# Kernel optimization log

Measured on AMD Instinct MI355X. Metric: run time of the kernel, lower is better.

## Reference

```python
import jax, jax.numpy as jnp
import numpy as np

N, D_IN, D_QK, D_V = 8192, 1024, 128, 128

def setup_inputs() -> dict:
    key = jax.random.key(0)
    k1, k2, k3, k4 = jax.random.split(key, 4)
    return {
        "x": jax.random.normal(k1, (N, D_IN), dtype=jnp.float32),
        "W_q": jax.random.normal(k2, (D_IN, D_QK), dtype=jnp.float32),
        "W_k": jax.random.normal(k3, (D_IN, D_QK), dtype=jnp.float32),
        "W_v": jax.random.normal(k4, (D_IN, D_V), dtype=jnp.float32),
    }

def reference(x, W_q, W_k, W_v):
    Q = x @ W_q          # [N, d_qk]
    K = x @ W_k          # [N, d_qk]
    V = x @ W_v          # [N, d_v]
    scale = 1.0 / jnp.sqrt(jnp.asarray(W_q.shape[1], dtype=Q.dtype))
    S = jnp.einsum("nd,md->nm", Q, K) * scale  # [N, N]
    A = jax.nn.softmax(S, axis=1)
    return A @ V         # [N, d_v]
```

## Files before the change

### kernel.cpp

```cpp
#include <hip/hip_runtime.h>
#include <cstdint>
#include <cstddef>

#define NTOK 8192
#define DIN  1024
#define DH   128
#define KVB  64

typedef __attribute__((ext_vector_type(4))) float f32x4;
typedef __bf16 bf16x8 __attribute__((ext_vector_type(8)));
typedef unsigned short u16x8 __attribute__((ext_vector_type(8)));
typedef unsigned short u16x4 __attribute__((ext_vector_type(4)));

__device__ __forceinline__ unsigned short f2bf(float f){
  union { float f; unsigned u; } x; x.f = f;
  unsigned r = x.u + 0x7FFFu + ((x.u >> 16) & 1u);
  return (unsigned short)(r >> 16);
}
__device__ __forceinline__ float bf2f(unsigned short b){
  union { unsigned u; float f; } x; x.u = ((unsigned)b) << 16;
  return x.f;
}
__device__ __forceinline__ void gload16(const void* g, void* l){
  using gp_t = const __attribute__((address_space(1))) char*;
  using lp_t = __attribute__((address_space(3))) char*;
  __builtin_amdgcn_global_load_lds((gp_t)(uintptr_t)g, (lp_t)(uint32_t)(uintptr_t)l, 16, 0, 0);
}

__global__ void k_wsplit(const float* __restrict__ Wq, const float* __restrict__ Wk,
                         const float* __restrict__ Wv,
                         unsigned short* __restrict__ WhT, unsigned short* __restrict__ WlT){
  int e = blockIdx.x * 256 + threadIdx.x;
  int n = e >> 10, k = e & 1023;
  const float* W = (n < 128) ? Wq : ((n < 256) ? Wk : Wv);
  float v = W[(size_t)k * 128 + (n & 127)];
  unsigned short h = f2bf(v);
  WhT[e] = h;
  WlT[e] = f2bf(v - bf2f(h));
}

__global__ void k_xsplit(const float* __restrict__ x,
                         unsigned short* __restrict__ xh, unsigned short* __restrict__ xl){
  size_t i = ((size_t)blockIdx.x * 256 + threadIdx.x) * 8;
  f32x4 a = *(const f32x4*)(x + i);
  f32x4 b = *(const f32x4*)(x + i + 4);
  u16x8 h, l;
  #pragma unroll
  for (int j = 0; j < 4; ++j){
    unsigned short h0 = f2bf(a[j]); h[j] = h0;   l[j]   = f2bf(a[j] - bf2f(h0));
    unsigned short h1 = f2bf(b[j]); h[4+j] = h1; l[4+j] = f2bf(b[j] - bf2f(h1));
  }
  *(u16x8*)(xh + i) = h;
  *(u16x8*)(xl + i) = l;
}

__global__ __launch_bounds__(256, 3) void k_proj(
    const unsigned short* __restrict__ xh, const unsigned short* __restrict__ xl,
    const unsigned short* __restrict__ WhT, const unsigned short* __restrict__ WlT,
    unsigned short* __restrict__ Qh, unsigned short* __restrict__ Ql,
    unsigned short* __restrict__ Kh, unsigned short* __restrict__ Kl,
    unsigned short* __restrict__ Vt){
  __shared__ __align__(16) char smem[32768];
  const int lane = threadIdx.x & 63, wid = threadIdx.x >> 6;
  const int l15 = lane & 15, lk = lane >> 4;
  const int bm = blockIdx.x;
  const int by = blockIdx.y;
  const int bt = by >> 1, nh = by & 1;
  const int wm = wid >> 1, wn = wid & 1;

  const int srow = lane >> 3;
  const int gc8  = (lane & 7) ^ srow;
  const unsigned short* gsrc;
  char* ldst;
  int grow0;
  if (wid == 0){      gsrc = xh;  grow0 = bm*64;            ldst = smem; }
  else if (wid == 1){ gsrc = xl;  grow0 = bm*64;            ldst = smem + 8192; }
  else if (wid == 2){ gsrc = WhT; grow0 = bt*128 + nh*64;   ldst = smem + 16384; }
  else {              gsrc = WlT; grow0 = bt*128 + nh*64;   ldst = smem + 24576; }
  const unsigned short* gbase = gsrc + (size_t)(grow0 + srow)*DIN + gc8*8;
  const bool stage_on = (bt < 2) || (wid == 0) || (wid == 2);

  f32x4 acc[2][2] = {};

  for (int t = 0; t < 16; ++t){
    if (stage_on){
      #pragma unroll
      for (int i = 0; i < 8; ++i)
        gload16(gbase + (size_t)i*8*DIN + t*64, ldst + i*1024);
    }
    __syncthreads();

    bf16x8 a_h[2][2], a_l[2][2], b_h[2][2], b_l[2][2];
    const unsigned sw = (unsigned)(l15 & 7);
    #pragma unroll
    for (int mf = 0; mf < 2; ++mf)
      #pragma unroll
      for (int kc = 0; kc < 2; ++kc){
        unsigned rA = (unsigned)(wm*32 + mf*16 + l15);
        unsigned offA = rA*128u + ((((unsigned)(kc*4 + lk)) ^ sw)*16u);
        a_h[mf][kc] = *(const bf16x8*)(const void*)(smem + offA);
        unsigned rB = (unsigned)(wn*32 + mf*16 + l15);
        unsigned offB = rB*128u + ((((unsigned)(kc*4 + lk)) ^ sw)*16u);
        b_h[mf][kc] = *(const bf16x8*)(const void*)(smem + 16384 + offB);
        if (bt < 2){
          a_l[mf][kc] = *(const bf16x8*)(const void*)(smem + 8192 + offA);
          b_l[mf][kc] = *(const bf16x8*)(const void*)(smem + 24576 + offB);
        }
      }
    #pragma unroll
    for (int mf = 0; mf < 2; ++mf)
      #pragma unroll
      for (int nf = 0; nf < 2; ++nf)
        #pragma unroll
        for (int kc = 0; kc < 2; ++kc){
          acc[mf][nf] = __builtin_amdgcn_mfma_f32_16x16x32_bf16(a_h[mf][kc], b_h[nf][kc], acc[mf][nf], 0,0,0);
          if (bt < 2){
            acc[mf][nf] = __builtin_amdgcn_mfma_f32_16x16x32_bf16(a_h[mf][kc], b_l[nf][kc], acc[mf][nf], 0,0,0);
            acc[mf][nf] = __builtin_amdgcn_mfma_f32_16x16x32_bf16(a_l[mf][kc], b_h[nf][kc], acc[mf][nf], 0,0,0);
          }
        }
    __syncthreads();
  }

  const float qscale = 0.08838834764831845f;
  #pragma unroll
  for (int mf = 0; mf < 2; ++mf){
    #pragma unroll
    for (int nf = 0; nf < 2; ++nf){
      #pragma unroll
      for (int r = 0; r < 4; ++r){
        int row = bm*64 + wm*32 + mf*16 + lk*4 + r;
        int col = nh*64 + wn*32 + nf*16 + l15;
        float v = acc[mf][nf][r];
        if (bt == 0){
          v *= qscale;
          unsigned short h = f2bf(v);
          Qh[(size_t)row*DH + col] = h;
          Ql[(size_t)row*DH + col] = f2bf(v - bf2f(h));
        } else if (bt == 1){
          unsigned short h = f2bf(v);
          Kh[(size_t)row*DH + col] = h;
          Kl[(size_t)row*DH + col] = f2bf(v - bf2f(h));
        } else {
          Vt[(size_t)col*NTOK + row] = f2bf(v);
        }
      }
    }
  }
}

__global__ __launch_bounds__(512, 4) void k_flash(
    const unsigned short* __restrict__ Qh, const unsigned short* __restrict__ Ql,
    const unsigned short* __restrict__ Kh, const unsigned short* __restrict__ Kl,
    const unsigned short* __restrict__ Vt,
    float* __restrict__ Opart, float* __restrict__ mpart, float* __restrict__ lpart,
    int ksplit){
  __shared__ __align__(16) char smem[65536];
  const int tid = threadIdx.x;
  const int lane = tid & 63, wid = tid >> 6;
  const int l15 = lane & 15, lk = lane >> 4;
  const int qb = blockIdx.x / ksplit, ks = blockIdx.x - qb*ksplit;
  const int q0 = qb*128 + wid*16;
  const int kvlen = NTOK / ksplit;
  const int kvbase = ks * kvlen;
  const int NT = kvlen / KVB;

  char* Pbase = smem + 48*1024 + wid*2048;

  bf16x8 qh[4], ql[4];
  #pragma unroll
  for (int kc = 0; kc < 4; ++kc){
    size_t off = (size_t)(q0 + l15)*DH + kc*32 + lk*8;
    qh[kc] = *(const bf16x8*)(const void*)(Qh + off);
    ql[kc] = *(const bf16x8*)(const void*)(Ql + off);
  }

  const int i0 = 2*wid, i1 = 2*wid + 1;
  int rk0 = 4*i0 + (lane >> 4), rk1 = 4*i1 + (lane >> 4);
  int gk0 = rk0*DH + ((lane & 15) ^ (rk0 & 7))*8;
  int gk1 = rk1*DH + ((lane & 15) ^ (rk1 & 7))*8;
  int rv0 = 8*i0 + (lane >> 3), rv1 = 8*i1 + (lane >> 3);
  int gv0 = rv0*NTOK + ((lane & 7) ^ (rv0 & 7))*8;
  int gv1 = rv1*NTOK + ((lane & 7) ^ (rv1 & 7))*8;
  char* ldsK0 = smem + i0*1024;
  char* ldsK1 = smem + i1*1024;

  #define STAGE(kv0_) do {                                              \
    int _o = (kv0_)*DH;                                                 \
    gload16(Kh + (size_t)(_o + gk0), ldsK0);                            \
    gload16(Kh + (size_t)(_o + gk1), ldsK1);                            \
    gload16(Kl + (size_t)(_o + gk0), ldsK0 + 16*1024);                  \
    gload16(Kl + (size_t)(_o + gk1), ldsK1 + 16*1024);                  \
    gload16(Vt + (size_t)(gv0 + (kv0_)), ldsK0 + 32*1024);              \
    gload16(Vt + (size_t)(gv1 + (kv0_)), ldsK1 + 32*1024);              \
  } while(0)

  STAGE(kvbase);
  __syncthreads();

  f32x4 o[8] = {};
  float m_run = -3.0e38f, l_run = 0.f;

  for (int t = 0; t < NT; ++t){
    f32x4 s[4] = {};
    __builtin_amdgcn_s_setprio(1);
    #pragma unroll
    for (int nf = 0; nf < 4; ++nf){
      const int row = nf*16 + l15;
      const unsigned rbase = (unsigned)row*256u;
      const unsigned sw = (unsigned)(row & 7);
      #pragma unroll
      for (int kc = 0; kc < 4; ++kc){
        unsigned boff = rbase + ((((unsigned)(kc*4 + lk)) ^ sw)*16u);
        bf16x8 khf = *(const bf16x8*)(const void*)(smem + boff);
        bf16x8 klf = *(const bf16x8*)(const void*)(smem + 16*1024 + boff);
        s[nf] = __builtin_amdgcn_mfma_f32_16x16x32_bf16(khf, qh[kc], s[nf], 0,0,0);
        s[nf] = __builtin_amdgcn_mfma_f32_16x16x32_bf16(klf, qh[kc], s[nf], 0,0,0);
        s[nf] = __builtin_amdgcn_mfma_f32_16x16x32_bf16(khf, ql[kc], s[nf], 0,0,0);
      }
    }
    __builtin_amdgcn_s_setprio(0);

    float mx = fmaxf(fmaxf(s[0][0], s[0][1]), fmaxf(s[0][2], s[0][3]));
    #pragma unroll
    for (int nf = 1; nf < 4; ++nf)
      mx = fmaxf(mx, fmaxf(fmaxf(s[nf][0], s[nf][1]), fmaxf(s[nf][2], s[nf][3])));
    mx = fmaxf(mx, __shfl_xor(mx, 16));
    mx = fmaxf(mx, __shfl_xor(mx, 32));
    float mnew = fmaxf(m_run, mx);
    float corr = __expf(m_run - mnew);
    float tsum = 0.f;
    #pragma unroll
    for (int nf = 0; nf < 4; ++nf){
      u16x4 pk;
      #pragma unroll
      for (int r = 0; r < 4; ++r){
        float p = __expf(s[nf][r] - mnew);
        tsum += p;
        pk[r] = f2bf(p);
      }
      *(u16x4*)(void*)(Pbase + l15*128 + (((unsigned)(nf*4 + lk)) ^ (2u*(unsigned)(l15 & 7)))*8u) = pk;
    }
    tsum += __shfl_xor(tsum, 16);
    tsum += __shfl_xor(tsum, 32);
    m_run = mnew;
    l_run = l_run*corr + tsum;
    #pragma unroll
    for (int nd = 0; nd < 8; ++nd) o[nd] *= corr;

    __builtin_amdgcn_s_setprio(1);
    #pragma unroll
    for (int kc2 = 0; kc2 < 2; ++kc2){
      bf16x8 pf = *(const bf16x8*)(const void*)(Pbase + l15*128 +
                    ((((unsigned)(kc2*4 + lk)) ^ (unsigned)(l15 & 7))*16u));
      #pragma unroll
      for (int nd = 0; nd < 8; ++nd){
        const int row = nd*16 + l15;
        unsigned boff = 32u*1024u + (unsigned)row*128u +
                        ((((unsigned)(kc2*4 + lk)) ^ (unsigned)(row & 7))*16u);
        bf16x8 vf = *(const bf16x8*)(const void*)(smem + boff);
        o[nd] = __builtin_amdgcn_mfma_f32_16x16x32_bf16(vf, pf, o[nd], 0,0,0);
      }
    }
    __builtin_amdgcn_s_setprio(0);

    __syncthreads();
    if (t + 1 < NT) STAGE(kvbase + (t+1)*KVB);
    __syncthreads();
  }
  #undef STAGE

  float* Op = Opart + ((size_t)ks*NTOK + q0 + l15)*DH;
  #pragma unroll
  for (int nd = 0; nd < 8; ++nd)
    *(f32x4*)(Op + nd*16 + lk*4) = o[nd];
  if (lk == 0){
    mpart[(size_t)ks*NTOK + q0 + l15] = m_run;
    lpart[(size_t)ks*NTOK + q0 + l15] = l_run;
  }
}

__global__ void k_merge(const float* __restrict__ Opart, const float* __restrict__ mpart,
                        const float* __restrict__ lpart, float* __restrict__ out, int ksplit){
  int gid = blockIdx.x*256 + threadIdx.x;
  int n = gid >> 5, c4 = (gid & 31) * 4;
  float M = -1e30f;
  for (int ks = 0; ks < ksplit; ++ks) M = fmaxf(M, mpart[(size_t)ks*NTOK + n]);
  float L = 0.f;
  f32x4 acc = {0.f, 0.f, 0.f, 0.f};
  for (int ks = 0; ks < ksplit; ++ks){
    float w = __expf(mpart[(size_t)ks*NTOK + n] - M);
    L += lpart[(size_t)ks*NTOK + n] * w;
    f32x4 op = *(const f32x4*)(Opart + ((size_t)ks*NTOK + n)*DH + c4);
    acc += op * w;
  }
  float inv = 1.f / L;
  *(f32x4*)(out + (size_t)n*DH + c4) = acc * inv;
}

extern "C" void kernel_launch(void* const* d_in, const int* in_sizes, int n_in,
                              void* d_out, int out_size, void* d_ws, size_t ws_size,
                              hipStream_t stream){
  const float* x  = (const float*)d_in[0];
  const float* Wq = (const float*)d_in[1];
  const float* Wk = (const float*)d_in[2];
  const float* Wv = (const float*)d_in[3];
  float* out = (float*)d_out;

  char* ws = (char*)d_ws;
  const size_t SZ_WT = (size_t)384*1024*2;
  const size_t SZ_X  = (size_t)NTOK*DIN*2;
  const size_t SZ_QK = (size_t)NTOK*DH*2;
  size_t off = 0;
  unsigned short* WhT = (unsigned short*)(ws + off); off += SZ_WT;
  unsigned short* WlT = (unsigned short*)(ws + off); off += SZ_WT;
  unsigned short* xh  = (unsigned short*)(ws + off); off += SZ_X;
  unsigned short* xl  = (unsigned short*)(ws + off); off += SZ_X;
  unsigned short* Qh  = (unsigned short*)(ws + off); off += SZ_QK;
  unsigned short* Ql  = (unsigned short*)(ws + off); off += SZ_QK;
  unsigned short* Kh  = (unsigned short*)(ws + off); off += SZ_QK;
  unsigned short* Kl  = (unsigned short*)(ws + off); off += SZ_QK;
  unsigned short* Vt  = (unsigned short*)(ws + off); off += SZ_QK;

  int ksplit = 8;
  while (ksplit > 1 &&
         off + (size_t)ksplit*(NTOK*(size_t)DH*4 + 2*NTOK*4) > ws_size)
    ksplit >>= 1;
  float* Opart = (float*)(ws + off); off += (size_t)ksplit*NTOK*DH*4;
  float* mpart = (float*)(ws + off); off += (size_t)ksplit*NTOK*4;
  float* lpart = (float*)(ws + off); off += (size_t)ksplit*NTOK*4;

  k_wsplit<<<dim3((384*1024)/256), dim3(256), 0, stream>>>(Wq, Wk, Wv, WhT, WlT);
  k_xsplit<<<dim3((NTOK*DIN)/(256*8)), dim3(256), 0, stream>>>(x, xh, xl);
  k_proj  <<<dim3(NTOK/64, 6), dim3(256), 0, stream>>>(xh, xl, WhT, WlT, Qh, Ql, Kh, Kl, Vt);
  k_flash <<<dim3((NTOK/128)*ksplit), dim3(512), 0, stream>>>(Qh, Ql, Kh, Kl, Vt,
                                                              Opart, mpart, lpart, ksplit);
  k_merge <<<dim3(NTOK*32/256), dim3(256), 0, stream>>>(Opart, mpart, lpart, out, ksplit);
}
```

Before: 181.6 us.

## Rework flash kernel to 32x32 MFMA tiles with register-resident P and lazy rescaling

The attention kernel now has 4 waves of 32 query rows each (256 threads) and uses 32x32x16 bf16 MFMAs in place of 16x16x32. The P tile stays in registers, packed with v_cvt_pk_bf16 and exchanged across half-waves with shuffles, so the LDS round trip for P is gone. Rescaling of the running max is skipped unless the new max exceeds the old by more than 8. This reduces LDS traffic and instruction count, but adds register pressure (f32x16 accumulators, 16 Q fragments), lowers occupancy, and relies on the threshold to keep exp values within range.

```diff
diff --git a/kernel.cpp b/kernel.cpp
--- a/kernel.cpp
+++ b/kernel.cpp
@@ -8,9 +8,10 @@
 #define KVB  64
 
 typedef __attribute__((ext_vector_type(4))) float f32x4;
+typedef __attribute__((ext_vector_type(16))) float f32x16;
 typedef __bf16 bf16x8 __attribute__((ext_vector_type(8)));
 typedef unsigned short u16x8 __attribute__((ext_vector_type(8)));
-typedef unsigned short u16x4 __attribute__((ext_vector_type(4)));
+typedef unsigned int u32x4 __attribute__((ext_vector_type(4)));
 
 __device__ __forceinline__ unsigned short f2bf(float f){
   union { float f; unsigned u; } x; x.f = f;
@@ -20,6 +21,11 @@
 __device__ __forceinline__ float bf2f(unsigned short b){
   union { unsigned u; float f; } x; x.u = ((unsigned)b) << 16;
   return x.f;
+}
+__device__ __forceinline__ unsigned cvtpk_bf16(float lo, float hi){
+  unsigned r;
+  asm volatile("v_cvt_pk_bf16_f32 %0, %1, %2" : "=v"(r) : "v"(lo), "v"(hi));
+  return r;
 }
 __device__ __forceinline__ void gload16(const void* g, void* l){
   using gp_t = const __attribute__((address_space(1))) char*;
@@ -149,117 +155,128 @@
   }
 }
 
-__global__ __launch_bounds__(512, 4) void k_flash(
+__global__ __launch_bounds__(256, 2) void k_flash(
     const unsigned short* __restrict__ Qh, const unsigned short* __restrict__ Ql,
     const unsigned short* __restrict__ Kh, const unsigned short* __restrict__ Kl,
     const unsigned short* __restrict__ Vt,
     float* __restrict__ Opart, float* __restrict__ mpart, float* __restrict__ lpart,
     int ksplit){
-  __shared__ __align__(16) char smem[65536];
+  __shared__ __align__(16) char smem[49152];
+  char* smemc = smem;
   const int tid = threadIdx.x;
   const int lane = tid & 63, wid = tid >> 6;
-  const int l15 = lane & 15, lk = lane >> 4;
+  const int l31 = lane & 31, hi = lane >> 5;
   const int qb = blockIdx.x / ksplit, ks = blockIdx.x - qb*ksplit;
-  const int q0 = qb*128 + wid*16;
+  const int q0w = qb*128 + wid*32;
   const int kvlen = NTOK / ksplit;
   const int kvbase = ks * kvlen;
   const int NT = kvlen / KVB;
 
-  char* Pbase = smem + 48*1024 + wid*2048;
-
-  bf16x8 qh[4], ql[4];
-  #pragma unroll
-  for (int kc = 0; kc < 4; ++kc){
-    size_t off = (size_t)(q0 + l15)*DH + kc*32 + lk*8;
+  bf16x8 qh[8], ql[8];
+  #pragma unroll
+  for (int kc = 0; kc < 8; ++kc){
+    size_t off = (size_t)(q0w + l31)*DH + kc*16 + hi*8;
     qh[kc] = *(const bf16x8*)(const void*)(Qh + off);
     ql[kc] = *(const bf16x8*)(const void*)(Ql + off);
   }
 
-  const int i0 = 2*wid, i1 = 2*wid + 1;
-  int rk0 = 4*i0 + (lane >> 4), rk1 = 4*i1 + (lane >> 4);
-  int gk0 = rk0*DH + ((lane & 15) ^ (rk0 & 7))*8;
-  int gk1 = rk1*DH + ((lane & 15) ^ (rk1 & 7))*8;
-  int rv0 = 8*i0 + (lane >> 3), rv1 = 8*i1 + (lane >> 3);
-  int gv0 = rv0*NTOK + ((lane & 7) ^ (rv0 & 7))*8;
-  int gv1 = rv1*NTOK + ((lane & 7) ^ (rv1 & 7))*8;
-  char* ldsK0 = smem + i0*1024;
-  char* ldsK1 = smem + i1*1024;
-
-  #define STAGE(kv0_) do {                                              \
-    int _o = (kv0_)*DH;                                                 \
-    gload16(Kh + (size_t)(_o + gk0), ldsK0);                            \
-    gload16(Kh + (size_t)(_o + gk1), ldsK1);                            \
-    gload16(Kl + (size_t)(_o + gk0), ldsK0 + 16*1024);                  \
-    gload16(Kl + (size_t)(_o + gk1), ldsK1 + 16*1024);                  \
-    gload16(Vt + (size_t)(gv0 + (kv0_)), ldsK0 + 32*1024);              \
-    gload16(Vt + (size_t)(gv1 + (kv0_)), ldsK1 + 32*1024);              \
-  } while(0)
+  int gK[4], gV[4], ldsO[4];
+  #pragma unroll
+  for (int i = 0; i < 4; ++i){
+    int g = 4*wid + i;
+    int rk = 4*g + (lane >> 4);
+    gK[i] = rk*DH + (((lane & 15) ^ (rk & 7))*8);
+    int rv = 8*g + (lane >> 3);
+    gV[i] = rv*NTOK + (((lane & 7) ^ (lane >> 3))*8);
+    ldsO[i] = g*1024;
+  }
+
+  #define STAGE(kv0_) do { int _o = (kv0_)*DH;                          \
+    _Pragma("unroll")                                                   \
+    for (int i = 0; i < 4; ++i){                                        \
+      gload16(Kh + (size_t)(_o + gK[i]), smemc + ldsO[i]);              \
+      gload16(Kl + (size_t)(_o + gK[i]), smemc + 16384 + ldsO[i]);      \
+      gload16(Vt + (size_t)(gV[i] + (kv0_)), smemc + 32768 + ldsO[i]);  \
+    } } while(0)
 
   STAGE(kvbase);
   __syncthreads();
 
-  f32x4 o[8] = {};
+  f32x16 o[4] = {};
   float m_run = -3.0e38f, l_run = 0.f;
 
   for (int t = 0; t < NT; ++t){
-    f32x4 s[4] = {};
+    f32x16 s0 = {}, s1 = {};
     __builtin_amdgcn_s_setprio(1);
     #pragma unroll
-    for (int nf = 0; nf < 4; ++nf){
-      const int row = nf*16 + l15;
-      const unsigned rbase = (unsigned)row*256u;
-      const unsigned sw = (unsigned)(row & 7);
-      #pragma unroll
-      for (int kc = 0; kc < 4; ++kc){
-        unsigned boff = rbase + ((((unsigned)(kc*4 + lk)) ^ sw)*16u);
-        bf16x8 khf = *(const bf16x8*)(const void*)(smem + boff);
-        bf16x8 klf = *(const bf16x8*)(const void*)(smem + 16*1024 + boff);
-        s[nf] = __builtin_amdgcn_mfma_f32_16x16x32_bf16(khf, qh[kc], s[nf], 0,0,0);
-        s[nf] = __builtin_amdgcn_mfma_f32_16x16x32_bf16(klf, qh[kc], s[nf], 0,0,0);
-        s[nf] = __builtin_amdgcn_mfma_f32_16x16x32_bf16(khf, ql[kc], s[nf], 0,0,0);
-      }
+    for (int kc = 0; kc < 8; ++kc){
+      int r0 = l31;
+      unsigned off0 = (unsigned)r0*256u + ((((unsigned)(kc*2 + hi)) ^ (unsigned)(r0 & 7))*16u);
+      bf16x8 kh0 = *(const bf16x8*)(const void*)(smemc + off0);
+      bf16x8 kl0 = *(const bf16x8*)(const void*)(smemc + 16384 + off0);
+      s0 = __builtin_amdgcn_mfma_f32_32x32x16_bf16(kh0, qh[kc], s0, 0,0,0);
+      s0 = __builtin_amdgcn_mfma_f32_32x32x16_bf16(kl0, qh[kc], s0, 0,0,0);
+      s0 = __builtin_amdgcn_mfma_f32_32x32x16_bf16(kh0, ql[kc], s0, 0,0,0);
+      int r1 = 32 + l31;
+      unsigned off1 = (unsigned)r1*256u + ((((unsigned)(kc*2 + hi)) ^ (unsigned)(r1 & 7))*16u);
+      bf16x8 kh1 = *(const bf16x8*)(const void*)(smemc + off1);
+      bf16x8 kl1 = *(const bf16x8*)(const void*)(smemc + 16384 + off1);
+      s1 = __builtin_amdgcn_mfma_f32_32x32x16_bf16(kh1, qh[kc], s1, 0,0,0);
+      s1 = __builtin_amdgcn_mfma_f32_32x32x16_bf16(kl1, qh[kc], s1, 0,0,0);
+      s1 = __builtin_amdgcn_mfma_f32_32x32x16_bf16(kh1, ql[kc], s1, 0,0,0);
     }
     __builtin_amdgcn_s_setprio(0);
 
-    float mx = fmaxf(fmaxf(s[0][0], s[0][1]), fmaxf(s[0][2], s[0][3]));
-    #pragma unroll
-    for (int nf = 1; nf < 4; ++nf)
-      mx = fmaxf(mx, fmaxf(fmaxf(s[nf][0], s[nf][1]), fmaxf(s[nf][2], s[nf][3])));
-    mx = fmaxf(mx, __shfl_xor(mx, 16));
-    mx = fmaxf(mx, __shfl_xor(mx, 32));
-    float mnew = fmaxf(m_run, mx);
-    float corr = __expf(m_run - mnew);
+    float pmax = s0[0];
+    #pragma unroll
+    for (int i = 1; i < 16; ++i) pmax = fmaxf(pmax, s0[i]);
+    #pragma unroll
+    for (int i = 0; i < 16; ++i) pmax = fmaxf(pmax, s1[i]);
+    pmax = fmaxf(pmax, __shfl_xor(pmax, 32));
+    if (!__all(pmax - m_run <= 8.f)){
+      float mnew = fmaxf(m_run, pmax);
+      float corr = __expf(m_run - mnew);
+      l_run *= corr;
+      #pragma unroll
+      for (int dblk = 0; dblk < 4; ++dblk)
+        #pragma unroll
+        for (int i = 0; i < 16; ++i) o[dblk][i] *= corr;
+      m_run = mnew;
+    }
     float tsum = 0.f;
     #pragma unroll
-    for (int nf = 0; nf < 4; ++nf){
-      u16x4 pk;
-      #pragma unroll
-      for (int r = 0; r < 4; ++r){
-        float p = __expf(s[nf][r] - mnew);
-        tsum += p;
-        pk[r] = f2bf(p);
-      }
-      *(u16x4*)(void*)(Pbase + l15*128 + (((unsigned)(nf*4 + lk)) ^ (2u*(unsigned)(l15 & 7)))*8u) = pk;
-    }
-    tsum += __shfl_xor(tsum, 16);
+    for (int i = 0; i < 16; ++i){ s0[i] = __expf(s0[i] - m_run); tsum += s0[i]; }
+    #pragma unroll
+    for (int i = 0; i < 16; ++i){ s1[i] = __expf(s1[i] - m_run); tsum += s1[i]; }
     tsum += __shfl_xor(tsum, 32);
-    m_run = mnew;
-    l_run = l_run*corr + tsum;
-    #pragma unroll
-    for (int nd = 0; nd < 8; ++nd) o[nd] *= corr;
+    l_run += tsum;
 
     __builtin_amdgcn_s_setprio(1);
     #pragma unroll
-    for (int kc2 = 0; kc2 < 2; ++kc2){
-      bf16x8 pf = *(const bf16x8*)(const void*)(Pbase + l15*128 +
-                    ((((unsigned)(kc2*4 + lk)) ^ (unsigned)(l15 & 7))*16u));
-      #pragma unroll
-      for (int nd = 0; nd < 8; ++nd){
-        const int row = nd*16 + l15;
-        unsigned boff = 32u*1024u + (unsigned)row*128u +
-                        ((((unsigned)(kc2*4 + lk)) ^ (unsigned)(row & 7))*16u);
-        bf16x8 vf = *(const bf16x8*)(const void*)(smem + boff);
-        o[nd] = __builtin_amdgcn_mfma_f32_16x16x32_bf16(vf, pf, o[nd], 0,0,0);
+    for (int b = 0; b < 4; ++b){
+      f32x16 sv = (b & 2) ? s1 : s0;
+      const int base = 8*(b & 1);
+      unsigned w0 = cvtpk_bf16(sv[base+0], sv[base+1]);
+      unsigned w1 = cvtpk_bf16(sv[base+2], sv[base+3]);
+      unsigned w2 = cvtpk_bf16(sv[base+4], sv[base+5]);
+      unsigned w3 = cvtpk_bf16(sv[base+6], sv[base+7]);
+      unsigned sx0 = (unsigned)__shfl_xor((int)w0, 32);
+      unsigned sx1 = (unsigned)__shfl_xor((int)w1, 32);
+      unsigned sx2 = (unsigned)__shfl_xor((int)w2, 32);
+      unsigned sx3 = (unsigned)__shfl_xor((int)w3, 32);
+      u32x4 pw;
+      pw[0] = hi ? sx2 : w0;
+      pw[1] = hi ? sx3 : w1;
+      pw[2] = hi ? w2 : sx0;
+      pw[3] = hi ? w3 : sx1;
+      bf16x8 pB = __builtin_bit_cast(bf16x8, pw);
+      #pragma unroll
+      for (int dblk = 0; dblk < 4; ++dblk){
+        int rv = dblk*32 + l31;
+        unsigned offv = 32768u + (unsigned)rv*128u +
+                        ((((unsigned)(b*2 + hi)) ^ (unsigned)(rv & 7))*16u);
+        bf16x8 vf = *(const bf16x8*)(const void*)(smemc + offv);
+        o[dblk] = __builtin_amdgcn_mfma_f32_32x32x16_bf16(vf, pB, o[dblk], 0,0,0);
       }
     }
     __builtin_amdgcn_s_setprio(0);
@@ -270,13 +287,17 @@
   }
   #undef STAGE
 
-  float* Op = Opart + ((size_t)ks*NTOK + q0 + l15)*DH;
-  #pragma unroll
-  for (int nd = 0; nd < 8; ++nd)
-    *(f32x4*)(Op + nd*16 + lk*4) = o[nd];
-  if (lk == 0){
-    mpart[(size_t)ks*NTOK + q0 + l15] = m_run;
-    lpart[(size_t)ks*NTOK + q0 + l15] = l_run;
+  float* Op = Opart + ((size_t)ks*NTOK + q0w + l31)*DH;
+  #pragma unroll
+  for (int dblk = 0; dblk < 4; ++dblk)
+    #pragma unroll
+    for (int g = 0; g < 4; ++g){
+      f32x4 q4 = { o[dblk][4*g+0], o[dblk][4*g+1], o[dblk][4*g+2], o[dblk][4*g+3] };
+      *(f32x4*)(Op + dblk*32 + 8*g + 4*hi) = q4;
+    }
+  if (hi == 0){
+    mpart[(size_t)ks*NTOK + q0w + l31] = m_run;
+    lpart[(size_t)ks*NTOK + q0w + l31] = l_run;
   }
 }
 
@@ -333,7 +354,7 @@
   k_wsplit<<<dim3((384*1024)/256), dim3(256), 0, stream>>>(Wq, Wk, Wv, WhT, WlT);
   k_xsplit<<<dim3((NTOK*DIN)/(256*8)), dim3(256), 0, stream>>>(x, xh, xl);
   k_proj  <<<dim3(NTOK/64, 6), dim3(256), 0, stream>>>(xh, xl, WhT, WlT, Qh, Ql, Kh, Kl, Vt);
-  k_flash <<<dim3((NTOK/128)*ksplit), dim3(512), 0, stream>>>(Qh, Ql, Kh, Kl, Vt,
+  k_flash <<<dim3((NTOK/128)*ksplit), dim3(256), 0, stream>>>(Qh, Ql, Kh, Kl, Vt,
                                                               Opart, mpart, lpart, ksplit);
   k_merge <<<dim3(NTOK*32/256), dim3(256), 0, stream>>>(Opart, mpart, lpart, out, ksplit);
 }
```

Measured after the change: 184.0 us. Within noise of the previous version (+1.3%).
